# Kernel tuning notes

Hardware: AMD Instinct MI355X
Metric: run time of the kernel (lower is better)

Reference implementation:

```python
import math
import jax, jax.numpy as jnp
import numpy as np

B, L, C, H = 4, 2048, 1024, 16
D = C // H


def setup_inputs() -> dict:
    key = jax.random.key(0)
    k1, k2, k3 = jax.random.split(key, 3)
    x = jax.random.normal(k1, (B, L, C), dtype=jnp.float32)
    Wqkv = jax.random.normal(k2, (C, 3 * C), dtype=jnp.float32) * (1.0 / math.sqrt(C))
    bqkv = jax.random.normal(k3, (3 * C,), dtype=jnp.float32) * 0.02
    return {"x": x, "Wqkv": Wqkv, "bqkv": bqkv}


def reference(x, Wqkv, bqkv):
    b, l, c = x.shape
    h, d = H, c // H
    qkv = x @ Wqkv + bqkv                      # [B, L, 3C]
    q, k, v = jnp.split(qkv, 3, axis=-1)
    # [B, L, C] -> [B, H, L, D]
    q = q.reshape(b, l, h, d).transpose(0, 2, 1, 3)
    k = k.reshape(b, l, h, d).transpose(0, 2, 1, 3)
    v = v.reshape(b, l, h, d).transpose(0, 2, 1, 3)
    scale = 1.0 / math.sqrt(d)
    scores = jnp.einsum('bhld,bhmd->bhlm', q, k) * scale  # [B, H, L, L]
    causal = jnp.tril(jnp.ones((l, l), dtype=bool))       # [L, L]
    scores = jnp.where(causal[None, None, :, :], scores, -jnp.inf)
    attn = jax.nn.softmax(scores, axis=-1)
    y = jnp.einsum('bhlm,bhmd->bhld', attn, v)            # [B, H, L, D]
    y = y.transpose(0, 2, 1, 3).reshape(b, l, c)          # [B, L, C]
    return y
```

## Files before the change

### kernel.cpp

```cpp
#include <hip/hip_runtime.h>

#define L_SEQ 2048
#define CDIM  1024
#define NH    16
#define HD    64
#define NBH   64
#define KDIM  1024

typedef __attribute__((ext_vector_type(4))) float f32x4;
typedef __attribute__((ext_vector_type(8))) short s16x8;
typedef __attribute__((ext_vector_type(4))) short s16x4;

__device__ inline short f2bf(float f) {
  union { float f; unsigned u; } v; v.f = f;
  unsigned r = v.u + 0x7fffu + ((v.u >> 16) & 1u);
  return (short)(r >> 16);
}

__device__ inline f32x4 mfma16(s16x8 a, s16x8 b, f32x4 c) {
  return __builtin_amdgcn_mfma_f32_16x16x32_bf16(a, b, c, 0, 0, 0);
}

__device__ inline unsigned cvt_pk_bf16(float lo, float hi) {
  unsigned r;
  asm("v_cvt_pk_bf16_f32 %0, %1, %2" : "=v"(r) : "v"(lo), "v"(hi));
  return r;
}

__device__ inline void gload_lds16(const short* g, short* l) {
  __builtin_amdgcn_global_load_lds(
      (const __attribute__((address_space(1))) unsigned*)g,
      (__attribute__((address_space(3))) unsigned*)l, 16, 0, 0);
}

__global__ __launch_bounds__(256) void convert_f32_bf16(const float* __restrict__ in,
                                                        short* __restrict__ out) {
  int i = (blockIdx.x * 256 + threadIdx.x) * 4;
  typedef __attribute__((ext_vector_type(4))) float fv4;
  fv4 v = *(const fv4*)(in + i);
  s16x4 o;
  o[0] = f2bf(v[0]); o[1] = f2bf(v[1]); o[2] = f2bf(v[2]); o[3] = f2bf(v[3]);
  *(s16x4*)(out + i) = o;
}

__global__ __launch_bounds__(256) void transpose_w(const float* __restrict__ W,
                                                   short* __restrict__ Wt) {
  __shared__ float tile[64][65];
  int n0 = blockIdx.x * 64, k0 = blockIdx.y * 64;
  int tc = threadIdx.x & 63, tr = threadIdx.x >> 6;
#pragma unroll
  for (int i = 0; i < 16; ++i) {
    int r = i * 4 + tr;
    tile[r][tc] = W[(size_t)(k0 + r) * 3072 + n0 + tc];
  }
  __syncthreads();
#pragma unroll
  for (int i = 0; i < 16; ++i) {
    int r = i * 4 + tr;
    Wt[(size_t)(n0 + r) * 1024 + k0 + tc] = f2bf(tile[tc][r]);
  }
}

__global__ __launch_bounds__(256) void qkv_gemm(const short* __restrict__ A,
                                                const short* __restrict__ Bt,
                                                const float* __restrict__ bias,
                                                short* __restrict__ Qo,
                                                short* __restrict__ Ko,
                                                short* __restrict__ Vt) {
  __shared__ __align__(16) short As[128 * 64];
  __shared__ __align__(16) short Bs[128 * 64];
  const int t = threadIdx.x;
  const int lane = t & 63, wid = t >> 6;
  const int wm = wid >> 1, wn = wid & 1;
  const int lrow = lane & 15, lg = lane >> 4;
  const int tm = blockIdx.x * 128, tn = blockIdx.y * 128;

  const int srow = lane >> 3;
  const int schunk = (lane & 7) ^ srow;
  const int sw = lrow & 7;

  f32x4 acc[4][4];
#pragma unroll
  for (int i = 0; i < 4; ++i)
#pragma unroll
    for (int j = 0; j < 4; ++j) { acc[i][j][0]=0.f; acc[i][j][1]=0.f; acc[i][j][2]=0.f; acc[i][j][3]=0.f; }

  for (int kt = 0; kt < KDIM; kt += 64) {
    __syncthreads();
#pragma unroll
    for (int ii = 0; ii < 4; ++ii) {
      int row0 = wid * 32 + ii * 8;
      int rowg = row0 + srow;
      gload_lds16(A  + (size_t)(tm + rowg) * KDIM + kt + schunk * 8, &As[row0 * 64]);
      gload_lds16(Bt + (size_t)(tn + rowg) * KDIM + kt + schunk * 8, &Bs[row0 * 64]);
    }
    asm volatile("s_waitcnt vmcnt(0)" ::: "memory");
    __syncthreads();

    s16x8 af[4][2], bf[4][2];
#pragma unroll
    for (int i = 0; i < 4; ++i) {
      int row = wm * 64 + i * 16 + lrow;
      af[i][0] = *(const s16x8*)(As + row * 64 + ((lg)     ^ sw) * 8);
      af[i][1] = *(const s16x8*)(As + row * 64 + ((4 + lg) ^ sw) * 8);
    }
#pragma unroll
    for (int j = 0; j < 4; ++j) {
      int row = wn * 64 + j * 16 + lrow;
      bf[j][0] = *(const s16x8*)(Bs + row * 64 + ((lg)     ^ sw) * 8);
      bf[j][1] = *(const s16x8*)(Bs + row * 64 + ((4 + lg) ^ sw) * 8);
    }
#pragma unroll
    for (int i = 0; i < 4; ++i)
#pragma unroll
      for (int j = 0; j < 4; ++j) {
        acc[i][j] = mfma16(af[i][0], bf[j][0], acc[i][j]);
        acc[i][j] = mfma16(af[i][1], bf[j][1], acc[i][j]);
      }
  }

  const float QS = 0.125f * 1.4426950408889634f;
#pragma unroll
  for (int i = 0; i < 4; ++i)
#pragma unroll
    for (int j = 0; j < 4; ++j) {
      int n = tn + wn * 64 + j * 16 + lrow;
      float bv = bias[n];
      int s = n >> 10, rem = n & 1023;
      int h = rem >> 6, d = rem & 63;
#pragma unroll
      for (int r = 0; r < 4; ++r) {
        int m = tm + wm * 64 + i * 16 + lg * 4 + r;
        int b = m >> 11, l = m & 2047;
        float v = acc[i][j][r] + bv;
        if (s == 0) {
          Qo[((size_t)(b * NH + h) * L_SEQ + l) * HD + d] = f2bf(v * QS);
        } else if (s == 1) {
          Ko[((size_t)(b * NH + h) * L_SEQ + l) * HD + d] = f2bf(v);
        } else {
          Vt[((size_t)(b * NH + h) * HD + d) * L_SEQ + l] = f2bf(v);
        }
      }
    }
}

__global__ __launch_bounds__(256) void attn(const short* __restrict__ Q,
                                            const short* __restrict__ K,
                                            const short* __restrict__ Vt,
                                            float* __restrict__ out) {
  const int t = threadIdx.x, lane = t & 63, wid = t >> 6;
  const int lrow = lane & 15, lg = lane >> 4;
  const int n = blockIdx.x;
  const int xcd = n & 7, slot = n >> 3;
  const int bh = xcd * 8 + (slot >> 4);
  const int qp = slot & 15;
  const size_t bhoff = (size_t)bh * L_SEQ * HD;
  const short* Qb = Q + bhoff;
  const short* Kb = K + bhoff;
  const short* Vb = Vt + (size_t)bh * HD * L_SEQ;
  const int b = bh >> 4, h = bh & 15;
  const int src0 = lrow + ((lane & 16) << 1);
  const int src1 = src0 + 16;
  const bool hi_nf = (lg & 2) != 0;

#pragma unroll
  for (int tt = 0; tt < 2; ++tt) {
    const int qt = tt ? (31 - qp) : qp;
    const int q0 = qt * 64 + wid * 16;
    const int qi = q0 + lrow;

    s16x8 qf0 = *(const s16x8*)(Qb + (size_t)qi * HD + lg * 8);
    s16x8 qf1 = *(const s16x8*)(Qb + (size_t)qi * HD + 32 + lg * 8);

    f32x4 o[4];
#pragma unroll
    for (int dt = 0; dt < 4; ++dt) { o[dt][0]=0.f; o[dt][1]=0.f; o[dt][2]=0.f; o[dt][3]=0.f; }
    float mr = -1e30f, lr = 0.f;

    const int kvend = q0 + 16;
    for (int kv0 = 0; kv0 < kvend; kv0 += 64) {
      s16x8 vf[2][4];
#pragma unroll
      for (int ks = 0; ks < 2; ++ks)
#pragma unroll
        for (int dt = 0; dt < 4; ++dt)
          vf[ks][dt] = *(const s16x8*)(Vb + (size_t)(dt * 16 + lrow) * L_SEQ + kv0 + ks * 32 + lg * 8);

      f32x4 s[4];
#pragma unroll
      for (int nf = 0; nf < 4; ++nf) {
        f32x4 sv; sv[0]=0.f; sv[1]=0.f; sv[2]=0.f; sv[3]=0.f;
        const short* Krow = Kb + (size_t)(kv0 + nf * 16 + lrow) * HD;
        sv = mfma16(*(const s16x8*)(Krow + lg * 8), qf0, sv);
        sv = mfma16(*(const s16x8*)(Krow + 32 + lg * 8), qf1, sv);
        s[nf] = sv;
      }
      if (kv0 + 63 > q0) {
#pragma unroll
        for (int nf = 0; nf < 4; ++nf)
#pragma unroll
          for (int r = 0; r < 4; ++r)
            if (kv0 + nf * 16 + lg * 4 + r > qi) s[nf][r] = -INFINITY;
      }
      float mt = s[0][0];
#pragma unroll
      for (int nf = 0; nf < 4; ++nf)
#pragma unroll
        for (int r = 0; r < 4; ++r) mt = fmaxf(mt, s[nf][r]);
      mt = fmaxf(mt, __shfl_xor(mt, 16));
      mt = fmaxf(mt, __shfl_xor(mt, 32));
      float mn = fmaxf(mr, mt);
      float fr = exp2f(mr - mn);
      mr = mn;
      float ps = 0.f;
#pragma unroll
      for (int nf = 0; nf < 4; ++nf)
#pragma unroll
        for (int r = 0; r < 4; ++r) {
          float p = exp2f(s[nf][r] - mn);
          s[nf][r] = p; ps += p;
        }
      ps += __shfl_xor(ps, 16);
      ps += __shfl_xor(ps, 32);
      lr = lr * fr + ps;
#pragma unroll
      for (int dt = 0; dt < 4; ++dt) o[dt] *= fr;

      unsigned w0[4], w1[4];
#pragma unroll
      for (int nf = 0; nf < 4; ++nf) {
        w0[nf] = cvt_pk_bf16(s[nf][0], s[nf][1]);
        w1[nf] = cvt_pk_bf16(s[nf][2], s[nf][3]);
      }

#pragma unroll
      for (int ks = 0; ks < 2; ++ks) {
        int a0 = __shfl((int)w0[2 * ks],     src0);
        int a1 = __shfl((int)w0[2 * ks + 1], src0);
        int b0 = __shfl((int)w1[2 * ks],     src0);
        int b1 = __shfl((int)w1[2 * ks + 1], src0);
        int c0 = __shfl((int)w0[2 * ks],     src1);
        int c1 = __shfl((int)w0[2 * ks + 1], src1);
        int d0 = __shfl((int)w1[2 * ks],     src1);
        int d1 = __shfl((int)w1[2 * ks + 1], src1);
        union { int i[4]; s16x8 v; } pu;
        pu.i[0] = hi_nf ? a1 : a0;
        pu.i[1] = hi_nf ? b1 : b0;
        pu.i[2] = hi_nf ? c1 : c0;
        pu.i[3] = hi_nf ? d1 : d0;
#pragma unroll
        for (int dt = 0; dt < 4; ++dt)
          o[dt] = mfma16(vf[ks][dt], pu.v, o[dt]);
      }
    }

    const float inv = 1.0f / lr;
    const size_t obase = (size_t)(b * L_SEQ + qi) * CDIM + h * HD + lg * 4;
#pragma unroll
    for (int dt = 0; dt < 4; ++dt) {
      f32x4 ov = o[dt] * inv;
      *(f32x4*)(out + obase + dt * 16) = ov;
    }
  }
}

extern "C" void kernel_launch(void* const* d_in, const int* in_sizes, int n_in,
                              void* d_out, int out_size, void* d_ws, size_t ws_size,
                              hipStream_t stream) {
  const float* x    = (const float*)d_in[0];
  const float* W    = (const float*)d_in[1];
  const float* bqkv = (const float*)d_in[2];
  float* out = (float*)d_out;
  char* ws = (char*)d_ws;

  const size_t SZ_XB  = (size_t)8192 * 1024 * 2;
  const size_t SZ_WT  = (size_t)3072 * 1024 * 2;
  const size_t SZ_HEAD = (size_t)NBH * L_SEQ * HD * 2;

  short* xb  = (short*)ws;
  short* wtb = (short*)(ws + SZ_XB);
  short* Qo  = (short*)(ws + SZ_XB + SZ_WT);
  short* Ko  = (short*)(ws + SZ_XB + SZ_WT + SZ_HEAD);
  short* Vtb = (short*)(ws + SZ_XB + SZ_WT + 2 * SZ_HEAD);

  convert_f32_bf16<<<8192, 256, 0, stream>>>(x, xb);
  transpose_w<<<dim3(48, 16), 256, 0, stream>>>(W, wtb);
  qkv_gemm<<<dim3(64, 24), 256, 0, stream>>>(xb, wtb, bqkv, Qo, Ko, Vtb);
  attn<<<1024, 256, 0, stream>>>(Qo, Ko, Vtb, out);
}
```

Baseline: 404.1 us.

## Split attention KV range across wave pairs and merge partial softmax via LDS

Each query group of 16 rows is now processed by two waves that take alternating 64-wide KV tiles, and their partial outputs and max/sum statistics are merged through shared memory at the end. The grid doubles to 2048 blocks and launch bounds request 8 blocks per SM, so more waves are in flight and each wave's serial KV loop is shorter. V fragments are now loaded per k-substep rather than all up front, which lowers register pressure. In exchange the kernel adds two block barriers, LDS traffic for the merge, and duplicate Q loads and softmax bookkeeping in both waves.

```diff
diff --git a/kernel.cpp b/kernel.cpp
--- a/kernel.cpp
+++ b/kernel.cpp
@@ -144,16 +144,17 @@
     }
 }
 
-__global__ __launch_bounds__(256) void attn(const short* __restrict__ Q,
-                                            const short* __restrict__ K,
-                                            const short* __restrict__ Vt,
-                                            float* __restrict__ out) {
+__global__ __launch_bounds__(256, 8) void attn(const short* __restrict__ Q,
+                                               const short* __restrict__ K,
+                                               const short* __restrict__ Vt,
+                                               float* __restrict__ out) {
+  __shared__ float mlds[2][64][20];
   const int t = threadIdx.x, lane = t & 63, wid = t >> 6;
   const int lrow = lane & 15, lg = lane >> 4;
   const int n = blockIdx.x;
   const int xcd = n & 7, slot = n >> 3;
-  const int bh = xcd * 8 + (slot >> 4);
-  const int qp = slot & 15;
+  const int bh = xcd * 8 + (slot >> 5);
+  const int p = slot & 31;
   const size_t bhoff = (size_t)bh * L_SEQ * HD;
   const short* Qb = Q + bhoff;
   const short* Kb = K + bhoff;
@@ -162,11 +163,13 @@
   const int src0 = lrow + ((lane & 16) << 1);
   const int src1 = src0 + 16;
   const bool hi_nf = (lg & 2) != 0;
+  const int gbase = 2 * p + (wid & 1);
 
 #pragma unroll
   for (int tt = 0; tt < 2; ++tt) {
-    const int qt = tt ? (31 - qp) : qp;
-    const int q0 = qt * 64 + wid * 16;
+    const int g = tt ? (127 - gbase) : gbase;
+    const int par = ((wid >> 1) ^ tt) & 1;
+    const int q0 = g * 16;
     const int qi = q0 + lrow;
 
     s16x8 qf0 = *(const s16x8*)(Qb + (size_t)qi * HD + lg * 8);
@@ -177,14 +180,9 @@
     for (int dt = 0; dt < 4; ++dt) { o[dt][0]=0.f; o[dt][1]=0.f; o[dt][2]=0.f; o[dt][3]=0.f; }
     float mr = -1e30f, lr = 0.f;
 
-    const int kvend = q0 + 16;
-    for (int kv0 = 0; kv0 < kvend; kv0 += 64) {
-      s16x8 vf[2][4];
-#pragma unroll
-      for (int ks = 0; ks < 2; ++ks)
-#pragma unroll
-        for (int dt = 0; dt < 4; ++dt)
-          vf[ks][dt] = *(const s16x8*)(Vb + (size_t)(dt * 16 + lrow) * L_SEQ + kv0 + ks * 32 + lg * 8);
+    const int T = (q0 + 16 + 63) >> 6;
+    for (int tile = par; tile < T; tile += 2) {
+      const int kv0 = tile * 64;
 
       f32x4 s[4];
 #pragma unroll
@@ -217,8 +215,8 @@
       for (int nf = 0; nf < 4; ++nf)
 #pragma unroll
         for (int r = 0; r < 4; ++r) {
-          float p = exp2f(s[nf][r] - mn);
-          s[nf][r] = p; ps += p;
+          float pp = exp2f(s[nf][r] - mn);
+          s[nf][r] = pp; ps += pp;
         }
       ps += __shfl_xor(ps, 16);
       ps += __shfl_xor(ps, 32);
@@ -235,6 +233,10 @@
 
 #pragma unroll
       for (int ks = 0; ks < 2; ++ks) {
+        s16x8 vf[4];
+#pragma unroll
+        for (int dt = 0; dt < 4; ++dt)
+          vf[dt] = *(const s16x8*)(Vb + (size_t)(dt * 16 + lrow) * L_SEQ + kv0 + ks * 32 + lg * 8);
         int a0 = __shfl((int)w0[2 * ks],     src0);
         int a1 = __shfl((int)w0[2 * ks + 1], src0);
         int b0 = __shfl((int)w1[2 * ks],     src0);
@@ -250,16 +252,32 @@
         pu.i[3] = hi_nf ? d1 : d0;
 #pragma unroll
         for (int dt = 0; dt < 4; ++dt)
-          o[dt] = mfma16(vf[ks][dt], pu.v, o[dt]);
-      }
-    }
-
-    const float inv = 1.0f / lr;
-    const size_t obase = (size_t)(b * L_SEQ + qi) * CDIM + h * HD + lg * 4;
-#pragma unroll
-    for (int dt = 0; dt < 4; ++dt) {
-      f32x4 ov = o[dt] * inv;
-      *(f32x4*)(out + obase + dt * 16) = ov;
+          o[dt] = mfma16(vf[dt], pu.v, o[dt]);
+      }
+    }
+
+    __syncthreads();
+    if (par) {
+      float* sm = &mlds[wid & 1][lane][0];
+#pragma unroll
+      for (int dt = 0; dt < 4; ++dt) *(f32x4*)(sm + dt * 4) = o[dt];
+      sm[16] = mr; sm[17] = lr;
+    }
+    __syncthreads();
+    if (!par) {
+      const float* sm = &mlds[wid & 1][lane][0];
+      float mb = sm[16], lb = sm[17];
+      float m = fmaxf(mr, mb);
+      float fa = exp2f(mr - m), fb = exp2f(mb - m);
+      float linv = 1.0f / (lr * fa + lb * fb);
+      fa *= linv; fb *= linv;
+      const size_t obase = (size_t)(b * L_SEQ + qi) * CDIM + h * HD + lg * 4;
+#pragma unroll
+      for (int dt = 0; dt < 4; ++dt) {
+        f32x4 ob = *(const f32x4*)(sm + dt * 4);
+        f32x4 ov = o[dt] * fa + ob * fb;
+        *(f32x4*)(out + obase + dt * 16) = ov;
+      }
     }
   }
 }
@@ -286,5 +304,5 @@
   convert_f32_bf16<<<8192, 256, 0, stream>>>(x, xb);
   transpose_w<<<dim3(48, 16), 256, 0, stream>>>(W, wtb);
   qkv_gemm<<<dim3(64, 24), 256, 0, stream>>>(xb, wtb, bqkv, Qo, Ko, Vtb);
-  attn<<<1024, 256, 0, stream>>>(Qo, Ko, Vtb, out);
-}
+  attn<<<2048, 256, 0, stream>>>(Qo, Ko, Vtb, out);
+}
```

New measurement: 492.8 us. 1.22x slower.
